# Performance work log

Hardware: AMD Instinct MI355X
Metric: run time of the kernel (lower is better)

The kernel has to match this reference:

```python
import jax, jax.numpy as jnp
import numpy as np


def setup_inputs() -> dict:
    key = jax.random.key(0)
    ks = jax.random.split(key, 7)
    B, I, H = 16384, 1024, 1024
    s = 1.0 / np.sqrt(H)
    return {
        "x": jax.random.normal(ks[0], (B, I), jnp.float32),
        "h_prev": jax.random.normal(ks[1], (B, H), jnp.float32),
        "c_prev": jax.random.normal(ks[2], (B, H), jnp.float32),
        "Wx": jax.random.normal(ks[3], (4, H, I), jnp.float32) * s,  # gates z,i,f,o
        "bx": jax.random.normal(ks[4], (4, H), jnp.float32) * s,
        "Rh": jax.random.normal(ks[5], (4, H, H), jnp.float32) * s,
        "bh": jax.random.normal(ks[6], (4, H), jnp.float32) * s,
    }


def reference(x, h_prev, c_prev, Wx, bx, Rh, bh):
    # Fused: 2 batched GEMMs for all 4 gates, then one elementwise block.
    # gates_x[g] = x @ Wx[g].T + bx[g]  (g in z,i,f,o), same for Rh/h_prev.
    gx = jnp.einsum('bi,ghi->gbh', x, Wx) + bx[:, None, :]       # [4,B,H]
    gh = jnp.einsum('bh,gkh->gbk', h_prev, Rh) + bh[:, None, :]  # [4,B,H]
    pre = gx + gh
    z = jnp.tanh(pre[0])
    i = jax.nn.sigmoid(pre[1])
    f = jax.nn.sigmoid(pre[2])
    o = jax.nn.sigmoid(pre[3])
    c = f * c_prev + i * z
    h = o * jnp.tanh(c)
    return (h, c)
```

## Files before the change

### kernel.cpp

```cpp
#include <hip/hip_runtime.h>
#include <stdint.h>

typedef __bf16 bf16;
typedef __bf16 bf16x4 __attribute__((ext_vector_type(4)));
typedef __bf16 bf16x8 __attribute__((ext_vector_type(8)));
typedef float  f32x4  __attribute__((ext_vector_type(4)));

#define B_DIM 16384
#define H_DIM 1024
#define K_DIM 2048

__device__ __forceinline__ void g2l16(const void* g, void* l) {
    __builtin_amdgcn_global_load_lds(
        (const __attribute__((address_space(1))) void*)g,
        (__attribute__((address_space(3))) void*)l,
        16, 0, 0);
}

__device__ __forceinline__ float sigm_fast(float x) {
    x = fminf(fmaxf(x, -40.f), 40.f);
    float e = __builtin_amdgcn_exp2f(-1.4426950408889634f * x);
    return __builtin_amdgcn_rcpf(1.0f + e);
}
__device__ __forceinline__ float tanh_fast(float x) {
    x = fminf(fmaxf(x, -40.f), 40.f);
    float e = __builtin_amdgcn_exp2f(-2.8853900817779268f * x);
    return (1.0f - e) * __builtin_amdgcn_rcpf(1.0f + e);
}

__global__ __launch_bounds__(256) void cvt_xh(const float* __restrict__ x,
                                              const float* __restrict__ h,
                                              bf16* __restrict__ U) {
    int t = blockIdx.x * 256 + threadIdx.x;
    int b = t >> 8;
    int j = (t & 255) << 2;
    float4 xv = *(const float4*)(x + ((size_t)b << 10) + j);
    float4 hv = *(const float4*)(h + ((size_t)b << 10) + j);
    bf16x4 xo = { (bf16)xv.x, (bf16)xv.y, (bf16)xv.z, (bf16)xv.w };
    bf16x4 ho = { (bf16)hv.x, (bf16)hv.y, (bf16)hv.z, (bf16)hv.w };
    *(bf16x4*)(U + ((size_t)b << 11) + j)        = xo;
    *(bf16x4*)(U + ((size_t)b << 11) + 1024 + j) = ho;
}

__global__ __launch_bounds__(256) void cvt_w(const float* __restrict__ Wx,
                                             const float* __restrict__ Rh,
                                             const float* __restrict__ bx,
                                             const float* __restrict__ bh,
                                             bf16* __restrict__ W,
                                             float* __restrict__ bb) {
    int t = blockIdx.x * 256 + threadIdx.x;
    int row = t >> 8;
    int col = (t & 255) << 2;
    float4 wv = *(const float4*)(Wx + ((size_t)row << 10) + col);
    float4 rv = *(const float4*)(Rh + ((size_t)row << 10) + col);
    bf16x4 wo = { (bf16)wv.x, (bf16)wv.y, (bf16)wv.z, (bf16)wv.w };
    bf16x4 ro = { (bf16)rv.x, (bf16)rv.y, (bf16)rv.z, (bf16)rv.w };
    *(bf16x4*)(W + ((size_t)row << 11) + col)        = wo;
    *(bf16x4*)(W + ((size_t)row << 11) + 1024 + col) = ro;
    if (t < 4096) bb[t] = bx[t] + bh[t];
}

__global__ __launch_bounds__(256, 2)
void lstm_fused(const bf16* __restrict__ U, const bf16* __restrict__ W,
                const float* __restrict__ bb, const float* __restrict__ cprev,
                float* __restrict__ out) {
    __shared__ __align__(16) bf16 As[128 * 64];
    __shared__ __align__(16) bf16 Bs[128 * 64];

    const int tid  = threadIdx.x;
    const int wave = tid >> 6;
    const int lane = tid & 63;
    const int quad = lane >> 4;
    const int lc   = lane & 15;

    int g   = blockIdx.x;
    int grp = g >> 8;
    int win = g & 255;
    int m_idx = (grp << 3) | (win & 7);
    int h_idx = win >> 3;
    const int m0 = m_idx << 7;
    const int h0 = h_idx << 5;

    float bias[2][4];
#pragma unroll
    for (int hi = 0; hi < 2; ++hi)
#pragma unroll
        for (int gg = 0; gg < 4; ++gg)
            bias[hi][gg] = bb[(gg << 10) + h0 + (hi << 4) + lc];

    f32x4 acc[2][8];
#pragma unroll
    for (int mi = 0; mi < 2; ++mi)
#pragma unroll
        for (int ni = 0; ni < 8; ++ni)
            acc[mi][ni] = (f32x4){0.f, 0.f, 0.f, 0.f};

    const char* Ub = (const char*)U;
    const char* Wb = (const char*)W;

    for (int kb = 0; kb < K_DIM / 64; ++kb) {
        __syncthreads();
#pragma unroll
        for (int s = 0; s < 4; ++s) {
            int off  = (s << 12) + (tid << 4);
            int row  = off >> 7;
            int colb = off & 127;
            int ldso = (s << 12) + (wave << 10);
            const char* ga = Ub + ((size_t)(m0 + row) << 12) + (kb << 7) + colb;
            g2l16(ga, (char*)As + ldso);
            int wrow = ((row >> 5) << 10) + h0 + (row & 31);
            const char* gb = Wb + ((size_t)wrow << 12) + (kb << 7) + colb;
            g2l16(gb, (char*)Bs + ldso);
        }
        __syncthreads();

#pragma unroll
        for (int ks = 0; ks < 2; ++ks) {
            bf16x8 af[2];
            bf16x8 bfr[8];
#pragma unroll
            for (int mi = 0; mi < 2; ++mi)
                af[mi] = *(const bf16x8*)(As + ((wave << 5) + (mi << 4) + lc) * 64 + (ks << 5) + (quad << 3));
#pragma unroll
            for (int ni = 0; ni < 8; ++ni)
                bfr[ni] = *(const bf16x8*)(Bs + ((ni << 4) + lc) * 64 + (ks << 5) + (quad << 3));
#pragma unroll
            for (int mi = 0; mi < 2; ++mi)
#pragma unroll
                for (int ni = 0; ni < 8; ++ni)
                    acc[mi][ni] = __builtin_amdgcn_mfma_f32_16x16x32_bf16(
                        af[mi], bfr[ni], acc[mi][ni], 0, 0, 0);
        }
    }

    float* out_h = out;
    float* out_c = out + (size_t)B_DIM * H_DIM;
#pragma unroll
    for (int mi = 0; mi < 2; ++mi) {
#pragma unroll
        for (int r = 0; r < 4; ++r) {
            int brow  = m0 + (wave << 5) + (mi << 4) + (quad << 2) + r;
            size_t rb = (size_t)brow << 10;
#pragma unroll
            for (int hi = 0; hi < 2; ++hi) {
                int h = h0 + (hi << 4) + lc;
                float zp = acc[mi][0 + hi][r] + bias[hi][0];
                float ip = acc[mi][2 + hi][r] + bias[hi][1];
                float fp = acc[mi][4 + hi][r] + bias[hi][2];
                float op = acc[mi][6 + hi][r] + bias[hi][3];
                float zz = tanh_fast(zp);
                float ii = sigm_fast(ip);
                float ff = sigm_fast(fp);
                float oo = sigm_fast(op);
                float cp = cprev[rb + h];
                float cn = ff * cp + ii * zz;
                float hn = oo * tanh_fast(cn);
                out_h[rb + h] = hn;
                out_c[rb + h] = cn;
            }
        }
    }
}

extern "C" void kernel_launch(void* const* d_in, const int* in_sizes, int n_in,
                              void* d_out, int out_size, void* d_ws, size_t ws_size,
                              hipStream_t stream) {
    const float* x  = (const float*)d_in[0];
    const float* hp = (const float*)d_in[1];
    const float* cp = (const float*)d_in[2];
    const float* Wx = (const float*)d_in[3];
    const float* bx = (const float*)d_in[4];
    const float* Rh = (const float*)d_in[5];
    const float* bh = (const float*)d_in[6];

    bf16*  U  = (bf16*)d_ws;
    bf16*  W  = (bf16*)((char*)d_ws + (size_t)67108864);
    float* bb = (float*)((char*)d_ws + (size_t)67108864 + 16777216);

    cvt_xh<<<16384, 256, 0, stream>>>(x, hp, U);
    cvt_w <<< 4096, 256, 0, stream>>>(Wx, Rh, bx, bh, W, bb);
    lstm_fused<<<4096, 256, 0, stream>>>(U, W, bb, cp, (float*)d_out);
}
```

Measured before the change: 621.7 us.

## Use 2x2 wave tiling, XOR-swizzled LDS, XCD-aware block mapping, and grid-stride conversion

The GEMM now splits the 128x128 tile into a 2x2 wave grid, where each wave computes 64x64 instead of 32x128. This changes how many A and B fragments each wave reads from LDS. LDS rows are XOR-swizzled by row to avoid bank conflicts on the fragment reads, and the B tile is interleaved so each wave's column half covers all four gates. Blocks are remapped so consecutive block ids spread across XCDs by h-tile, which aims to improve L2 reuse of weights. The conversion kernels switch to grid-stride loops with 16-byte bf16 stores.

Result: faster. 591.2 us (-4.9%).

```diff
diff --git a/kernel.cpp b/kernel.cpp
--- a/kernel.cpp
+++ b/kernel.cpp
@@ -2,7 +2,6 @@
 #include <stdint.h>
 
 typedef __bf16 bf16;
-typedef __bf16 bf16x4 __attribute__((ext_vector_type(4)));
 typedef __bf16 bf16x8 __attribute__((ext_vector_type(8)));
 typedef float  f32x4  __attribute__((ext_vector_type(4)));
 
@@ -31,15 +30,20 @@
 __global__ __launch_bounds__(256) void cvt_xh(const float* __restrict__ x,
                                               const float* __restrict__ h,
                                               bf16* __restrict__ U) {
-    int t = blockIdx.x * 256 + threadIdx.x;
-    int b = t >> 8;
-    int j = (t & 255) << 2;
-    float4 xv = *(const float4*)(x + ((size_t)b << 10) + j);
-    float4 hv = *(const float4*)(h + ((size_t)b << 10) + j);
-    bf16x4 xo = { (bf16)xv.x, (bf16)xv.y, (bf16)xv.z, (bf16)xv.w };
-    bf16x4 ho = { (bf16)hv.x, (bf16)hv.y, (bf16)hv.z, (bf16)hv.w };
-    *(bf16x4*)(U + ((size_t)b << 11) + j)        = xo;
-    *(bf16x4*)(U + ((size_t)b << 11) + 1024 + j) = ho;
+    const int NCH = (B_DIM * K_DIM) / 8;
+    int stride = gridDim.x * 256;
+    for (int i = blockIdx.x * 256 + threadIdx.x; i < NCH; i += stride) {
+        int row = i >> 8;
+        int c8  = i & 255;
+        const float* src = (c8 < 128)
+            ? (x + ((size_t)row << 10) + (c8 << 3))
+            : (h + ((size_t)row << 10) + ((c8 - 128) << 3));
+        float4 a = *(const float4*)src;
+        float4 b = *(const float4*)(src + 4);
+        bf16x8 o = { (bf16)a.x, (bf16)a.y, (bf16)a.z, (bf16)a.w,
+                     (bf16)b.x, (bf16)b.y, (bf16)b.z, (bf16)b.w };
+        *(bf16x8*)(U + ((size_t)i << 3)) = o;
+    }
 }
 
 __global__ __launch_bounds__(256) void cvt_w(const float* __restrict__ Wx,
@@ -48,16 +52,22 @@
                                              const float* __restrict__ bh,
                                              bf16* __restrict__ W,
                                              float* __restrict__ bb) {
-    int t = blockIdx.x * 256 + threadIdx.x;
-    int row = t >> 8;
-    int col = (t & 255) << 2;
-    float4 wv = *(const float4*)(Wx + ((size_t)row << 10) + col);
-    float4 rv = *(const float4*)(Rh + ((size_t)row << 10) + col);
-    bf16x4 wo = { (bf16)wv.x, (bf16)wv.y, (bf16)wv.z, (bf16)wv.w };
-    bf16x4 ro = { (bf16)rv.x, (bf16)rv.y, (bf16)rv.z, (bf16)rv.w };
-    *(bf16x4*)(W + ((size_t)row << 11) + col)        = wo;
-    *(bf16x4*)(W + ((size_t)row << 11) + 1024 + col) = ro;
-    if (t < 4096) bb[t] = bx[t] + bh[t];
+    const int NCH = (4096 * K_DIM) / 8;
+    int t0 = blockIdx.x * 256 + threadIdx.x;
+    int stride = gridDim.x * 256;
+    for (int i = t0; i < NCH; i += stride) {
+        int row = i >> 8;
+        int c8  = i & 255;
+        const float* src = (c8 < 128)
+            ? (Wx + ((size_t)row << 10) + (c8 << 3))
+            : (Rh + ((size_t)row << 10) + ((c8 - 128) << 3));
+        float4 a = *(const float4*)src;
+        float4 b = *(const float4*)(src + 4);
+        bf16x8 o = { (bf16)a.x, (bf16)a.y, (bf16)a.z, (bf16)a.w,
+                     (bf16)b.x, (bf16)b.y, (bf16)b.z, (bf16)b.w };
+        *(bf16x8*)(W + ((size_t)i << 3)) = o;
+    }
+    if (t0 < 4096) bb[t0] = bx[t0] + bh[t0];
 }
 
 __global__ __launch_bounds__(256, 2)
@@ -72,27 +82,27 @@
     const int lane = tid & 63;
     const int quad = lane >> 4;
     const int lc   = lane & 15;
+    const int wm   = wave >> 1;
+    const int wn   = wave & 1;
 
-    int g   = blockIdx.x;
-    int grp = g >> 8;
-    int win = g & 255;
-    int m_idx = (grp << 3) | (win & 7);
-    int h_idx = win >> 3;
+    int bid   = blockIdx.x;
+    int xcd   = bid & 7;
+    int j     = bid >> 3;
+    int h_idx = xcd + ((j >> 7) << 3);
+    int m_idx = j & 127;
     const int m0 = m_idx << 7;
     const int h0 = h_idx << 5;
 
-    float bias[2][4];
+    float bias[4];
 #pragma unroll
-    for (int hi = 0; hi < 2; ++hi)
+    for (int g = 0; g < 4; ++g)
+        bias[g] = bb[(g << 10) + h0 + (wn << 4) + lc];
+
+    f32x4 acc[4][4];
 #pragma unroll
-        for (int gg = 0; gg < 4; ++gg)
-            bias[hi][gg] = bb[(gg << 10) + h0 + (hi << 4) + lc];
-
-    f32x4 acc[2][8];
+    for (int mi = 0; mi < 4; ++mi)
 #pragma unroll
-    for (int mi = 0; mi < 2; ++mi)
-#pragma unroll
-        for (int ni = 0; ni < 8; ++ni)
+        for (int ni = 0; ni < 4; ++ni)
             acc[mi][ni] = (f32x4){0.f, 0.f, 0.f, 0.f};
 
     const char* Ub = (const char*)U;
@@ -102,32 +112,41 @@
         __syncthreads();
 #pragma unroll
         for (int s = 0; s < 4; ++s) {
-            int off  = (s << 12) + (tid << 4);
-            int row  = off >> 7;
-            int colb = off & 127;
-            int ldso = (s << 12) + (wave << 10);
+            int slot  = (s << 8) + (wave << 6) + lane;
+            int row   = slot >> 3;
+            int chunk = slot & 7;
+            int colb  = (chunk ^ (row & 7)) << 4;
+            int lb    = slot << 4;
             const char* ga = Ub + ((size_t)(m0 + row) << 12) + (kb << 7) + colb;
-            g2l16(ga, (char*)As + ldso);
-            int wrow = ((row >> 5) << 10) + h0 + (row & 31);
+            g2l16(ga, (char*)As + lb);
+            int gate = (row >> 4) & 3;
+            int hh   = ((row >> 6) << 4) + (row & 15);
+            int wrow = (gate << 10) + h0 + hh;
             const char* gb = Wb + ((size_t)wrow << 12) + (kb << 7) + colb;
-            g2l16(gb, (char*)Bs + ldso);
+            g2l16(gb, (char*)Bs + lb);
         }
         __syncthreads();
 
 #pragma unroll
         for (int ks = 0; ks < 2; ++ks) {
-            bf16x8 af[2];
-            bf16x8 bfr[8];
+            bf16x8 af[4];
+            bf16x8 bfr[4];
 #pragma unroll
-            for (int mi = 0; mi < 2; ++mi)
-                af[mi] = *(const bf16x8*)(As + ((wave << 5) + (mi << 4) + lc) * 64 + (ks << 5) + (quad << 3));
+            for (int mi = 0; mi < 4; ++mi) {
+                int row = (wm << 6) + (mi << 4) + lc;
+                int cs  = ((ks << 2) + quad) ^ (lc & 7);
+                af[mi]  = *(const bf16x8*)(As + (row << 6) + (cs << 3));
+            }
 #pragma unroll
-            for (int ni = 0; ni < 8; ++ni)
-                bfr[ni] = *(const bf16x8*)(Bs + ((ni << 4) + lc) * 64 + (ks << 5) + (quad << 3));
+            for (int ni = 0; ni < 4; ++ni) {
+                int row = (wn << 6) + (ni << 4) + lc;
+                int cs  = ((ks << 2) + quad) ^ (lc & 7);
+                bfr[ni] = *(const bf16x8*)(Bs + (row << 6) + (cs << 3));
+            }
 #pragma unroll
-            for (int mi = 0; mi < 2; ++mi)
+            for (int mi = 0; mi < 4; ++mi)
 #pragma unroll
-                for (int ni = 0; ni < 8; ++ni)
+                for (int ni = 0; ni < 4; ++ni)
                     acc[mi][ni] = __builtin_amdgcn_mfma_f32_16x16x32_bf16(
                         af[mi], bfr[ni], acc[mi][ni], 0, 0, 0);
         }
@@ -135,29 +154,26 @@
 
     float* out_h = out;
     float* out_c = out + (size_t)B_DIM * H_DIM;
+    const int h = h0 + (wn << 4) + lc;
 #pragma unroll
-    for (int mi = 0; mi < 2; ++mi) {
+    for (int mi = 0; mi < 4; ++mi) {
 #pragma unroll
         for (int r = 0; r < 4; ++r) {
-            int brow  = m0 + (wave << 5) + (mi << 4) + (quad << 2) + r;
+            int brow  = m0 + (wm << 6) + (mi << 4) + (quad << 2) + r;
             size_t rb = (size_t)brow << 10;
-#pragma unroll
-            for (int hi = 0; hi < 2; ++hi) {
-                int h = h0 + (hi << 4) + lc;
-                float zp = acc[mi][0 + hi][r] + bias[hi][0];
-                float ip = acc[mi][2 + hi][r] + bias[hi][1];
-                float fp = acc[mi][4 + hi][r] + bias[hi][2];
-                float op = acc[mi][6 + hi][r] + bias[hi][3];
-                float zz = tanh_fast(zp);
-                float ii = sigm_fast(ip);
-                float ff = sigm_fast(fp);
-                float oo = sigm_fast(op);
-                float cp = cprev[rb + h];
-                float cn = ff * cp + ii * zz;
-                float hn = oo * tanh_fast(cn);
-                out_h[rb + h] = hn;
-                out_c[rb + h] = cn;
-            }
+            float zp = acc[mi][0][r] + bias[0];
+            float ip = acc[mi][1][r] + bias[1];
+            float fp = acc[mi][2][r] + bias[2];
+            float op = acc[mi][3][r] + bias[3];
+            float zz = tanh_fast(zp);
+            float ii = sigm_fast(ip);
+            float ff = sigm_fast(fp);
+            float oo = sigm_fast(op);
+            float cp = cprev[rb + h];
+            float cn = ff * cp + ii * zz;
+            float hn = oo * tanh_fast(cn);
+            out_h[rb + h] = hn;
+            out_c[rb + h] = cn;
         }
     }
 }
@@ -177,7 +193,7 @@
     bf16*  W  = (bf16*)((char*)d_ws + (size_t)67108864);
     float* bb = (float*)((char*)d_ws + (size_t)67108864 + 16777216);
 
-    cvt_xh<<<16384, 256, 0, stream>>>(x, hp, U);
-    cvt_w <<< 4096, 256, 0, stream>>>(Wx, Rh, bx, bh, W, bb);
+    cvt_xh<<<2048, 256, 0, stream>>>(x, hp, U);
+    cvt_w <<<1024, 256, 0, stream>>>(Wx, Rh, bx, bh, W, bb);
     lstm_fused<<<4096, 256, 0, stream>>>(U, W, bb, cp, (float*)d_out);
 }
```
